# Kernel optimization log

Hardware: AMD Instinct MI355X
Metric: run time of the kernel (lower is better)

## Reference

```python
import jax, jax.numpy as jnp
import numpy as np

NUM_QUBITS = 12
NUM_LAYERS = 2
STATE_DIM = 2 ** NUM_QUBITS
BATCH = 4096
TWO_PI = 2 * 3.1416  # matches the original initializer constant


def _u3(theta, phi, lam):
    """Single-qubit U3 gate, 2x2 complex64 (matches TF layer exactly)."""
    c = jnp.cos(theta / 2)
    s = jnp.sin(theta / 2)
    z = jnp.zeros_like(phi)
    e_phi = jnp.exp(jax.lax.complex(z, phi))
    e_lam = jnp.exp(jax.lax.complex(z, lam))
    e_pl = jnp.exp(jax.lax.complex(z, phi + lam))
    cc = jax.lax.complex(c, jnp.zeros_like(c))
    sc = jax.lax.complex(s, jnp.zeros_like(s))
    row1 = jnp.stack([cc, -e_lam * sc])
    row2 = jnp.stack([e_phi * sc, e_pl * cc])
    return jnp.stack([row1, row2])  # [2, 2] complex64


def _full_gate(theta_vec, phi_vec, lam_vec):
    """Kronecker product of per-qubit gates -> [2^n, 2^n] complex64."""
    full = _u3(theta_vec[0], phi_vec[0], lam_vec[0])
    for q in range(1, theta_vec.shape[0]):
        full = jnp.kron(full, _u3(theta_vec[q], phi_vec[q], lam_vec[q]))
    return full


def setup_inputs() -> dict:
    key = jax.random.key(0)
    k1, k2, k3, k4 = jax.random.split(key, 4)
    inputs = jax.random.normal(k1, (BATCH, STATE_DIM), dtype=jnp.float32)
    thetas = jax.random.uniform(k2, (NUM_LAYERS, NUM_QUBITS), minval=0.0, maxval=TWO_PI, dtype=jnp.float32)
    phis = jax.random.uniform(k3, (NUM_LAYERS, NUM_QUBITS), minval=0.0, maxval=TWO_PI, dtype=jnp.float32)
    lams = jax.random.uniform(k4, (NUM_LAYERS, NUM_QUBITS), minval=0.0, maxval=TWO_PI, dtype=jnp.float32)
    return {"inputs": inputs, "thetas": thetas, "phis": phis, "lams": lams}


def reference(inputs, thetas, phis, lams):
    # normalize real inputs as complex state, per-sample L2 norm
    state = jax.lax.complex(inputs, jnp.zeros_like(inputs))  # [B, D] complex64
    norm = jnp.linalg.norm(state, axis=1, keepdims=True)      # real, [B, 1]
    state = state / norm
    for l in range(thetas.shape[0]):
        U = _full_gate(thetas[l], phis[l], lams[l])  # [D, D]
        # matvec(U, x) per sample == state @ U^T, batched GEMM replaces tf.map_fn
        state = state @ U.T
    return jnp.real(state * jnp.conj(state))  # probabilities, [B, D] float32
```

## Files before the change

### kernel.cpp

```cpp
#include <hip/hip_runtime.h>
#include <hip/hip_fp16.h>

#define NQ   12
#define DIM  4096
#define NL   2
#define BATCH 4096
#define SPB  8

typedef _Float16 half8  __attribute__((ext_vector_type(8)));
typedef float    f32x16 __attribute__((ext_vector_type(16)));
typedef __fp16   hv2    __attribute__((ext_vector_type(2)));


union U4H8 { uint4 u; half8 h; };

__device__ __forceinline__ unsigned pkrtz(float a, float b) {
    union { hv2 h; unsigned u; } c;
    c.h = __builtin_amdgcn_cvt_pkrtz(a, b);
    return c.u;
}

__global__ void build_gates(const float* __restrict__ th,
                            const float* __restrict__ ph,
                            const float* __restrict__ lm,
                            unsigned short* __restrict__ ws) {
    __shared__ float g[12][8];
    int t = threadIdx.x;
    if (t < NQ) {
        int q = t;
        float g00r = 1.f, g00i = 0.f, g01r = 0.f, g01i = 0.f;
        float g10r = 0.f, g10i = 0.f, g11r = 1.f, g11i = 0.f;
        #pragma unroll
        for (int l = 0; l < NL; ++l) {
            float th2 = 0.5f * th[l * NQ + q];
            float p   = ph[l * NQ + q];
            float la  = lm[l * NQ + q];
            float s, c, sl, cl, sp, cp, spl, cpl;
            sincosf(th2, &s, &c);
            sincosf(la, &sl, &cl);
            sincosf(p, &sp, &cp);
            sincosf(p + la, &spl, &cpl);
            float u00r = c,        u00i = 0.f;
            float u01r = -cl * s,  u01i = -sl * s;
            float u10r = cp * s,   u10i = sp * s;
            float u11r = cpl * c,  u11i = spl * c;
            float n00r = u00r*g00r - u00i*g00i + u01r*g10r - u01i*g10i;
            float n00i = u00r*g00i + u00i*g00r + u01r*g10i + u01i*g10r;
            float n01r = u00r*g01r - u00i*g01i + u01r*g11r - u01i*g11i;
            float n01i = u00r*g01i + u00i*g01r + u01r*g11i + u01i*g11r;
            float n10r = u10r*g00r - u10i*g00i + u11r*g10r - u11i*g10i;
            float n10i = u10r*g00i + u10i*g00r + u11r*g10i + u11i*g10r;
            float n11r = u10r*g01r - u10i*g01i + u11r*g11r - u11i*g11i;
            float n11i = u10r*g01i + u10i*g01r + u11r*g11i + u11i*g11r;
            g00r = n00r; g00i = n00i; g01r = n01r; g01i = n01i;
            g10r = n10r; g10i = n10i; g11r = n11r; g11i = n11i;
        }
        g[q][0] = g00r; g[q][1] = g00i; g[q][2] = g01r; g[q][3] = g01i;
        g[q][4] = g10r; g[q][5] = g10i; g[q][6] = g11r; g[q][7] = g11i;
    }
    __syncthreads();

    {
        int idx  = blockIdx.x * 256 + t;
        int arr  = idx >> 13;
        int rem  = idx & 8191;
        int frag = rem >> 9;
        int lane = (rem >> 3) & 63;
        int j    = rem & 7;
        int row, col, base, k, nn = 0;
        if (arr == 0) {
            int n4 = frag >> 2, ks = frag & 3;
            nn  = n4 * 32 + (lane & 31);
            k   = ks * 16 + ((lane >> 5) << 3) + j;
            row = nn & 63; col = k; base = 6;
        } else {
            int m = frag >> 3, ks = frag & 7;
            row = m * 32 + (lane & 31);
            k   = ks * 16 + ((lane >> 5) << 3) + j;
            col = k & 63; base = 0;
        }
        float re = 1.f, im = 0.f;
        #pragma unroll
        for (int qq = 0; qq < 6; ++qq) {
            const float* G = g[base + qq];
            int rb = (row >> (5 - qq)) & 1;
            int cb = (col >> (5 - qq)) & 1;
            float fr = G[rb * 4 + cb * 2], fi = G[rb * 4 + cb * 2 + 1];
            float nre = re * fr - im * fi;
            float nim = re * fi + im * fr;
            re = nre; im = nim;
        }
        float val;
        if (arr == 0)      val = (nn < 64) ? re : im;
        else if (arr == 1) val = (k < 64) ? re : -im;
        else               val = (k < 64) ? im :  re;
        union { __fp16 h; unsigned short s; } cv;
        cv.h = (__fp16)val;
        ws[idx] = cv.s;
    }
}

__global__ __launch_bounds__(256, 2)
void qc_sim(const float* __restrict__ in,
            const unsigned short* __restrict__ gw,
            float* __restrict__ out) {
    __shared__ unsigned Xh32[2048];
    __shared__ unsigned Tc32[4096];
    __shared__ float red[4];

    const int t = threadIdx.x, lane = t & 63, w = t >> 6, b = blockIdx.x;
    const int m1 = w & 1, ng = (w >> 1) * 2;
    const int m2 = w & 1, n2 = w >> 1;

    const uint4* __restrict__ wsv = reinterpret_cast<const uint4*>(gw);
    uint4 g1b[2][4], m1f[8], m2f[8];
    #pragma unroll
    for (int n = 0; n < 2; ++n)
        #pragma unroll
        for (int ks = 0; ks < 4; ++ks)
            g1b[n][ks] = wsv[((ng + n) * 4 + ks) * 64 + lane];
    #pragma unroll
    for (int ks = 0; ks < 8; ++ks) m1f[ks] = wsv[1024 + (m2 * 8 + ks) * 64 + lane];
    #pragma unroll
    for (int ks = 0; ks < 8; ++ks) m2f[ks] = wsv[2048 + (m2 * 8 + ks) * 64 + lane];

    const float* __restrict__ base_in  = in  + (size_t)b * SPB * DIM;
    float*       __restrict__ base_out = out + (size_t)b * SPB * DIM;

    float4 cur[4], nxt[4];
    {
        const float4* __restrict__ x4 = reinterpret_cast<const float4*>(base_in);
        #pragma unroll
        for (int j = 0; j < 4; ++j) cur[j] = x4[j * 256 + t];
    }

    for (int s = 0; s < SPB; ++s) {
        float ss = 0.f;
        #pragma unroll
        for (int j = 0; j < 4; ++j)
            ss += cur[j].x*cur[j].x + cur[j].y*cur[j].y
                + cur[j].z*cur[j].z + cur[j].w*cur[j].w;
        #pragma unroll
        for (int off = 32; off > 0; off >>= 1) ss += __shfl_down(ss, off, 64);
        if (lane == 0) red[w] = ss;

        #pragma unroll
        for (int j = 0; j < 4; ++j) {
            int fi = (j * 256 + t) * 4, r = fi >> 6, c = fi & 63;
            int a32 = r * 32 + ((((c >> 3) ^ (r & 7)) << 2)) + ((c & 7) >> 1);
            Xh32[a32]     = pkrtz(cur[j].x, cur[j].y);
            Xh32[a32 + 1] = pkrtz(cur[j].z, cur[j].w);
        }
        if (s + 1 < SPB) {
            const float4* __restrict__ xn =
                reinterpret_cast<const float4*>(base_in + (size_t)(s + 1) * DIM);
            #pragma unroll
            for (int j = 0; j < 4; ++j) nxt[j] = xn[j * 256 + t];
        }
        __syncthreads();
        const float inv = 1.0f / (red[0] + red[1] + red[2] + red[3]);

        f32x16 acc0 = {0,0,0,0,0,0,0,0,0,0,0,0,0,0,0,0};
        f32x16 acc1 = {0,0,0,0,0,0,0,0,0,0,0,0,0,0,0,0};
        const int rowX = m1 * 32 + (lane & 31);
        #pragma unroll
        for (int ks = 0; ks < 4; ++ks) {
            int kb  = ks * 16 + ((lane >> 5) << 3);
            int a32 = rowX * 32 + ((((kb >> 3) ^ (rowX & 7)) << 2));
            U4H8 xf; xf.u = *reinterpret_cast<const uint4*>(&Xh32[a32]);
            U4H8 b0; b0.u = g1b[0][ks];
            U4H8 b1; b1.u = g1b[1][ks];
            acc0 = __builtin_amdgcn_mfma_f32_32x32x16_f16(xf.h, b0.h, acc0, 0, 0, 0);
            acc1 = __builtin_amdgcn_mfma_f32_32x32x16_f16(xf.h, b1.h, acc1, 0, 0, 0);
        }

        #pragma unroll
        for (int tile = 0; tile < 2; ++tile) {
            int nt = ng + tile;
            const f32x16& acc = tile ? acc1 : acc0;
            int kofs = m1 * 32 + 64 * (nt >> 1) + ((lane >> 5) << 2);
            int cc   = (nt & 1) * 32 + (lane & 31);
            #pragma unroll
            for (int p = 0; p < 4; ++p) {
                int k0  = kofs + p * 8;
                int a32 = cc * 64 + (((k0 >> 3) ^ (cc & 15)) << 2) + ((k0 & 7) >> 1);
                Tc32[a32]     = pkrtz(acc[4 * p],     acc[4 * p + 1]);
                Tc32[a32 + 1] = pkrtz(acc[4 * p + 2], acc[4 * p + 3]);
            }
        }
        __syncthreads();

        f32x16 accR = {0,0,0,0,0,0,0,0,0,0,0,0,0,0,0,0};
        f32x16 accI = {0,0,0,0,0,0,0,0,0,0,0,0,0,0,0,0};
        const int cT = n2 * 32 + (lane & 31);
        #pragma unroll
        for (int ks = 0; ks < 8; ++ks) {
            int kb  = ks * 16 + ((lane >> 5) << 3);
            int a32 = cT * 64 + (((kb >> 3) ^ (cT & 15)) << 2);
            U4H8 tf; tf.u = *reinterpret_cast<const uint4*>(&Tc32[a32]);
            U4H8 a1; a1.u = m1f[ks];
            U4H8 a2; a2.u = m2f[ks];
            accR = __builtin_amdgcn_mfma_f32_32x32x16_f16(a1.h, tf.h, accR, 0, 0, 0);
            accI = __builtin_amdgcn_mfma_f32_32x32x16_f16(a2.h, tf.h, accI, 0, 0, 0);
        }

        float* __restrict__ o = base_out + (size_t)s * DIM
            + (size_t)((m2 * 32 + ((lane >> 5) << 2)) * 64 + n2 * 32 + (lane & 31));
        #pragma unroll
        for (int r = 0; r < 16; ++r) {
            int off = ((r & 3) + 8 * (r >> 2)) * 64;
            o[off] = (accR[r] * accR[r] + accI[r] * accI[r]) * inv;
        }

        if (s + 1 < SPB) {
            #pragma unroll
            for (int j = 0; j < 4; ++j) cur[j] = nxt[j];
        }
    }
}

extern "C" void kernel_launch(void* const* d_in, const int* in_sizes, int n_in,
                              void* d_out, int out_size, void* d_ws, size_t ws_size,
                              hipStream_t stream) {
    (void)in_sizes; (void)n_in; (void)out_size; (void)ws_size;
    const float* inputs = (const float*)d_in[0];
    const float* thetas = (const float*)d_in[1];
    const float* phis   = (const float*)d_in[2];
    const float* lams   = (const float*)d_in[3];
    unsigned short* gates = (unsigned short*)d_ws;
    float* out = (float*)d_out;

    hipLaunchKernelGGL(build_gates, dim3(96), dim3(256), 0, stream,
                       thetas, phis, lams, gates);
    hipLaunchKernelGGL(qc_sim, dim3(BATCH / SPB), dim3(256), 0, stream,
                       inputs, gates, out);
}
```

Baseline: 123.5 us.

## Halve second-stage gate fragments via complex sign trick, raise occupancy, shrink samples per block

The second-stage gate matrix is now stored as separate real and imaginary 64x64 halves instead of a packed 128-wide complex form. The negated imaginary part is produced on the fly by flipping fp16 sign bits, which halves the per-thread register fragments for that stage. The freed registers allow launch bounds to rise from 2 to 3 blocks per SM, and samples per block drop from 8 to 4 so there are twice as many blocks. In exchange there is a little extra XOR work per MFMA, and each block spends more of its time loading gate fragments relative to the samples it processes.

```diff
diff --git a/kernel.cpp b/kernel.cpp
--- a/kernel.cpp
+++ b/kernel.cpp
@@ -5,7 +5,7 @@
 #define DIM  4096
 #define NL   2
 #define BATCH 4096
-#define SPB  8
+#define SPB  4
 
 typedef _Float16 half8  __attribute__((ext_vector_type(8)));
 typedef float    f32x16 __attribute__((ext_vector_type(16)));
@@ -62,8 +62,8 @@
 
     {
         int idx  = blockIdx.x * 256 + t;
-        int arr  = idx >> 13;
-        int rem  = idx & 8191;
+        int arr  = (idx < 8192) ? 0 : (idx < 12288 ? 1 : 2);
+        int rem  = idx - (arr == 0 ? 0 : (arr == 1 ? 8192 : 12288));
         int frag = rem >> 9;
         int lane = (rem >> 3) & 63;
         int j    = rem & 7;
@@ -74,10 +74,10 @@
             k   = ks * 16 + ((lane >> 5) << 3) + j;
             row = nn & 63; col = k; base = 6;
         } else {
-            int m = frag >> 3, ks = frag & 7;
+            int m = frag >> 2, ks = frag & 3;
             row = m * 32 + (lane & 31);
             k   = ks * 16 + ((lane >> 5) << 3) + j;
-            col = k & 63; base = 0;
+            col = k; base = 0;
         }
         float re = 1.f, im = 0.f;
         #pragma unroll
@@ -92,15 +92,15 @@
         }
         float val;
         if (arr == 0)      val = (nn < 64) ? re : im;
-        else if (arr == 1) val = (k < 64) ? re : -im;
-        else               val = (k < 64) ? im :  re;
+        else if (arr == 1) val = re;
+        else               val = im;
         union { __fp16 h; unsigned short s; } cv;
         cv.h = (__fp16)val;
         ws[idx] = cv.s;
     }
 }
 
-__global__ __launch_bounds__(256, 2)
+__global__ __launch_bounds__(256, 3)
 void qc_sim(const float* __restrict__ in,
             const unsigned short* __restrict__ gw,
             float* __restrict__ out) {
@@ -113,16 +113,16 @@
     const int m2 = w & 1, n2 = w >> 1;
 
     const uint4* __restrict__ wsv = reinterpret_cast<const uint4*>(gw);
-    uint4 g1b[2][4], m1f[8], m2f[8];
+    uint4 g1b[2][4], brf[4], bif[4];
     #pragma unroll
     for (int n = 0; n < 2; ++n)
         #pragma unroll
         for (int ks = 0; ks < 4; ++ks)
             g1b[n][ks] = wsv[((ng + n) * 4 + ks) * 64 + lane];
     #pragma unroll
-    for (int ks = 0; ks < 8; ++ks) m1f[ks] = wsv[1024 + (m2 * 8 + ks) * 64 + lane];
+    for (int ks = 0; ks < 4; ++ks) brf[ks] = wsv[1024 + (m2 * 4 + ks) * 64 + lane];
     #pragma unroll
-    for (int ks = 0; ks < 8; ++ks) m2f[ks] = wsv[2048 + (m2 * 8 + ks) * 64 + lane];
+    for (int ks = 0; ks < 4; ++ks) bif[ks] = wsv[1536 + (m2 * 4 + ks) * 64 + lane];
 
     const float* __restrict__ base_in  = in  + (size_t)b * SPB * DIM;
     float*       __restrict__ base_out = out + (size_t)b * SPB * DIM;
@@ -194,14 +194,27 @@
         f32x16 accI = {0,0,0,0,0,0,0,0,0,0,0,0,0,0,0,0};
         const int cT = n2 * 32 + (lane & 31);
         #pragma unroll
-        for (int ks = 0; ks < 8; ++ks) {
+        for (int ks = 0; ks < 4; ++ks) {
             int kb  = ks * 16 + ((lane >> 5) << 3);
             int a32 = cT * 64 + (((kb >> 3) ^ (cT & 15)) << 2);
-            U4H8 tf; tf.u = *reinterpret_cast<const uint4*>(&Tc32[a32]);
-            U4H8 a1; a1.u = m1f[ks];
-            U4H8 a2; a2.u = m2f[ks];
-            accR = __builtin_amdgcn_mfma_f32_32x32x16_f16(a1.h, tf.h, accR, 0, 0, 0);
-            accI = __builtin_amdgcn_mfma_f32_32x32x16_f16(a2.h, tf.h, accI, 0, 0, 0);
+            U4H8 tr; tr.u = *reinterpret_cast<const uint4*>(&Tc32[a32]);
+            U4H8 br; br.u = brf[ks];
+            U4H8 bi; bi.u = bif[ks];
+            accR = __builtin_amdgcn_mfma_f32_32x32x16_f16(br.h, tr.h, accR, 0, 0, 0);
+            accI = __builtin_amdgcn_mfma_f32_32x32x16_f16(bi.h, tr.h, accI, 0, 0, 0);
+        }
+        #pragma unroll
+        for (int ks = 4; ks < 8; ++ks) {
+            int kb  = ks * 16 + ((lane >> 5) << 3);
+            int a32 = cT * 64 + (((kb >> 3) ^ (cT & 15)) << 2);
+            U4H8 ti; ti.u = *reinterpret_cast<const uint4*>(&Tc32[a32]);
+            U4H8 br; br.u = brf[ks - 4];
+            uint4 nb = bif[ks - 4];
+            nb.x ^= 0x80008000u; nb.y ^= 0x80008000u;
+            nb.z ^= 0x80008000u; nb.w ^= 0x80008000u;
+            U4H8 nbi; nbi.u = nb;
+            accR = __builtin_amdgcn_mfma_f32_32x32x16_f16(nbi.h, ti.h, accR, 0, 0, 0);
+            accI = __builtin_amdgcn_mfma_f32_32x32x16_f16(br.h,  ti.h, accI, 0, 0, 0);
         }
 
         float* __restrict__ o = base_out + (size_t)s * DIM
@@ -230,7 +243,7 @@
     unsigned short* gates = (unsigned short*)d_ws;
     float* out = (float*)d_out;
 
-    hipLaunchKernelGGL(build_gates, dim3(96), dim3(256), 0, stream,
+    hipLaunchKernelGGL(build_gates, dim3(64), dim3(256), 0, stream,
                        thetas, phis, lams, gates);
     hipLaunchKernelGGL(qc_sim, dim3(BATCH / SPB), dim3(256), 0, stream,
                        inputs, gates, out);
```

After: 130.1 us. 5.3% more time.
